# Optimization experiments

Measured on AMD Instinct MI355X. Metric: run time of the kernel, lower is better.

## Reference

```python
import jax, jax.numpy as jnp
import numpy as np

K = 2  # top-k experts per token

def setup_inputs() -> dict:
    key = jax.random.key(0)
    ks = jax.random.split(key, 4)
    B, D, E, H = 8192, 512, 8, 2048
    x = jax.random.normal(ks[0], (B, D), dtype=jnp.float32)
    w_gate = jax.random.normal(ks[1], (D, E), dtype=jnp.float32) * 0.02
    W1 = jax.random.normal(ks[2], (E, D, H), dtype=jnp.float32) * (1.0 / np.sqrt(D))
    b1 = jnp.zeros((E, H), dtype=jnp.float32)
    W2 = jax.random.normal(ks[3], (E, H, D), dtype=jnp.float32) * (1.0 / np.sqrt(H))
    b2 = jnp.zeros((E, D), dtype=jnp.float32)
    return {"x": x, "w_gate": w_gate, "W1": W1, "b1": b1, "W2": W2, "b2": b2}

def reference(x, w_gate, W1, b1, W2, b2):
    B, E = x.shape[0], w_gate.shape[1]
    # --- gating (eval path: clean logits, no noise) ---
    logits = x @ w_gate                                  # [B, E]
    top_vals, top_idx = jax.lax.top_k(logits, K)         # [B, K]
    top_gates = jax.nn.softmax(top_vals, axis=-1)        # softmax over top-k logits
    rows = jnp.arange(B)[:, None]
    gates = jnp.zeros((B, E), dtype=x.dtype).at[rows, top_idx].set(top_gates)  # [B, E]
    # --- expert MLPs (grouped GEMMs) ---
    h = jax.nn.gelu(jnp.einsum('bd,edh->beh', x, W1) + b1[None], approximate=False)  # [B, E, H]
    out = jnp.einsum('beh,ehd->bed', h, W2) + b2[None]   # [B, E, D]
    # --- combine weighted by sparse gates ---
    y = jnp.einsum('be,bed->bd', gates, out)             # [B, D]
    return y
```

## Files before the change

### kernel.cpp

```cpp
#include <hip/hip_runtime.h>
#include <cstdint>

#define B_TOK 8192
#define DIM   512
#define NEXP  8
#define HID   2048

#define BM 128
#define BN 128
#define BK 64
#define BN2 64
#define MAXTILES (B_TOK * 2 / BM + NEXP)
#define MPX 17
#define PAD_SLOTS (MAXTILES * BM)

typedef float  floatx4 __attribute__((ext_vector_type(4)));
typedef __bf16 bf16x8  __attribute__((ext_vector_type(8)));

__device__ __forceinline__ unsigned short f2bf(float f){
  unsigned u = __float_as_uint(f);
  u += 0x7fffu + ((u >> 16) & 1u);
  return (unsigned short)(u >> 16);
}

__device__ __forceinline__ float bf2f(unsigned short u){
  return __uint_as_float((unsigned)u << 16);
}

__device__ __forceinline__ float erf_fast(float x){
  float ax = fabsf(x);
  float t  = 1.0f / (1.0f + 0.3275911f * ax);
  float p  = t * (0.254829592f + t * (-0.284496736f + t * (1.421413741f +
             t * (-1.453152027f + t * 1.061405429f))));
  float r  = 1.0f - p * __expf(-ax * ax);
  return copysignf(r, x);
}

__device__ __forceinline__ float gelu_fast(float v){
  return 0.5f * v * (1.0f + erf_fast(v * 0.70710678118654752440f));
}

__device__ __forceinline__ void async_load16(const void* g, void* l){
  __builtin_amdgcn_global_load_lds(
      (__attribute__((address_space(1))) unsigned int*)const_cast<void*>(g),
      (__attribute__((address_space(3))) unsigned int*)l, 16, 0, 0);
}


__global__ void k_cvt_x(const float* __restrict__ x, unsigned short* __restrict__ xb){
  int i = blockIdx.x * blockDim.x + threadIdx.x;
  float4 v = ((const float4*)x)[i];
  ushort4 o;
  o.x = f2bf(v.x); o.y = f2bf(v.y); o.z = f2bf(v.z); o.w = f2bf(v.w);
  ((ushort4*)xb)[i] = o;
}

__global__ __launch_bounds__(256)
void k_transpose_bf16(const float* __restrict__ src, unsigned short* __restrict__ dst,
                      int R, int C){
  __shared__ unsigned short tile[64][65];
  const size_t eoff = (size_t)blockIdx.z * (size_t)R * (size_t)C;
  const float* s = src + eoff;
  unsigned short* d = dst + eoff;
  int r0 = blockIdx.y * 64, c0 = blockIdx.x * 64;
  int tr = threadIdx.x >> 4, tc = threadIdx.x & 15;
  #pragma unroll
  for (int i = 0; i < 4; i++){
    int r = tr + i * 16;
    float4 v = *(const float4*)(s + (size_t)(r0 + r) * C + c0 + tc * 4);
    tile[tc*4+0][r] = f2bf(v.x);
    tile[tc*4+1][r] = f2bf(v.y);
    tile[tc*4+2][r] = f2bf(v.z);
    tile[tc*4+3][r] = f2bf(v.w);
  }
  __syncthreads();
  #pragma unroll
  for (int i = 0; i < 4; i++){
    int rr = tr + i * 16;
    ushort4 o;
    o.x = tile[rr][tc*4+0]; o.y = tile[rr][tc*4+1];
    o.z = tile[rr][tc*4+2]; o.w = tile[rr][tc*4+3];
    *(ushort4*)(d + (size_t)(c0 + rr) * R + r0 + tc * 4) = o;
  }
}

__global__ __launch_bounds__(256)
void k_gate(const float* __restrict__ x, const float* __restrict__ wg,
            int* __restrict__ tidx, float* __restrict__ tgate){
  const int wave = threadIdx.x >> 6, lane = threadIdx.x & 63;
  const int t = blockIdx.x * 4 + wave;
  const float* xr = x + (size_t)t * DIM;
  double acc[8];
  #pragma unroll
  for (int e = 0; e < 8; e++) acc[e] = 0.0;
  for (int d = lane; d < DIM; d += 64){
    double xv = (double)xr[d];
    float4 a = *(const float4*)(wg + d * 8);
    float4 b = *(const float4*)(wg + d * 8 + 4);
    acc[0] += xv * (double)a.x; acc[1] += xv * (double)a.y;
    acc[2] += xv * (double)a.z; acc[3] += xv * (double)a.w;
    acc[4] += xv * (double)b.x; acc[5] += xv * (double)b.y;
    acc[6] += xv * (double)b.z; acc[7] += xv * (double)b.w;
  }
  #pragma unroll
  for (int off = 32; off > 0; off >>= 1){
    #pragma unroll
    for (int e = 0; e < 8; e++)
      acc[e] += __shfl_down(acc[e], off);
  }
  if (lane == 0){
    int i0 = 0; double v0 = acc[0];
    #pragma unroll
    for (int e = 1; e < 8; e++) if (acc[e] > v0){ v0 = acc[e]; i0 = e; }
    int i1 = -1; double v1 = -1e300;
    #pragma unroll
    for (int e = 0; e < 8; e++) if (e != i0 && acc[e] > v1){ v1 = acc[e]; i1 = e; }
    double g0 = 1.0 / (1.0 + exp(v1 - v0));
    tidx[2*t]   = i0; tidx[2*t+1] = i1;
    tgate[2*t]  = (float)g0;
    tgate[2*t+1]= (float)(1.0 - g0);
  }
}

__global__ __launch_bounds__(1024)
void k_count(const int* __restrict__ tidx, int* __restrict__ ctrl,
             int2* __restrict__ tmap){
  __shared__ int hist[16][8];
  const int tid = threadIdx.x;
  const int wave = tid >> 6;
  if (tid < 128) ((int*)hist)[tid] = 0;
  __syncthreads();
  #pragma unroll
  for (int i = 0; i < 8; i++){
    int t = i * 1024 + tid;
    int2 e = ((const int2*)tidx)[t];
    atomicAdd(&hist[wave][e.x], 1);
    atomicAdd(&hist[wave][e.y], 1);
  }
  __syncthreads();
  if (tid == 0){
    int o = 0, nt = 0;
    for (int e = 0; e < 8; e++){
      int c = 0;
      for (int w = 0; w < 16; w++) c += hist[w][e];
      ctrl[e] = c; ctrl[8 + e] = o; ctrl[16 + e] = o;
      int tiles = (c + BM - 1) / BM;
      for (int tk = 0; tk < tiles; tk++) tmap[nt++] = make_int2(e, tk * BM);
      o += tiles * BM;
    }
    for (; nt < MAXTILES; nt++) tmap[nt] = make_int2(0, 1 << 30);
  }
}

__global__ __launch_bounds__(256)
void k_place(const int* __restrict__ tidx, int* __restrict__ ctrl,
             int* __restrict__ perm, int2* __restrict__ slotpos){
  __shared__ int cnt[8];
  __shared__ int base[8];
  const int tid = threadIdx.x;
  if (tid < 8) cnt[tid] = 0;
  __syncthreads();
  const int t = blockIdx.x * 256 + tid;
  const int e0 = tidx[2*t], e1 = tidx[2*t+1];
  const int r0 = atomicAdd(&cnt[e0], 1);
  const int r1 = atomicAdd(&cnt[e1], 1);
  __syncthreads();
  if (tid < 8) base[tid] = atomicAdd(&ctrl[16 + tid], cnt[tid]);
  __syncthreads();
  const int p0 = base[e0] + r0, p1 = base[e1] + r1;
  perm[p0] = t;
  perm[p1] = t;
  slotpos[t] = make_int2(p0, p1);
}


__global__ __launch_bounds__(256, 4)
void k_gemm1(const unsigned short* __restrict__ xb,
             const unsigned short* __restrict__ w1t,
             const float* __restrict__ b1,
             unsigned short* __restrict__ h,
             const int* __restrict__ perm,
             const int* __restrict__ ctrl,
             const int2* __restrict__ tmap){
  const int xcd = blockIdx.x & 7;
  const int g   = blockIdx.x >> 3;
  const int nti = g & 15;
  const int mi  = g >> 4;
  const int2 tm = tmap[xcd * MPX + mi];
  const int e = tm.x;
  const int m0 = tm.y;
  const int count = ctrl[e];
  if (m0 >= count) return;
  const int hoff = ctrl[8 + e];
  const int n0 = nti * BN;

  __shared__ unsigned short smem[BM*BK + BN*BK + 2048];
  unsigned short* As = smem;
  unsigned short* Bs = smem + BM*BK;

  const int tid  = threadIdx.x;
  const int wave = tid >> 6;
  const int lane = tid & 63;
  const int rl   = wave * 32 + (lane >> 3);
  const int swz  = (lane & 7) ^ ((lane >> 3) & 7);

  const unsigned short* agp[4];
  const unsigned short* bgp[4];
  const unsigned short* w1e = w1t + (size_t)e * HID * DIM;
  #pragma unroll
  for (int i = 0; i < 4; i++){
    int srow = perm[hoff + m0 + rl + i * 8];
    agp[i] = xb + (size_t)srow * DIM + swz * 8;
    bgp[i] = w1e + (size_t)(n0 + rl + i * 8) * DIM + swz * 8;
  }
  unsigned short* asw = As + (wave * 32) * BK + lane * 8;
  unsigned short* bsw = Bs + (wave * 32) * BK + lane * 8;

  const int mh = (wave & 1) * 64;
  const int nh = (wave >> 1) * 64;
  const int fr = lane & 15;
  const int fq = lane >> 4;

  floatx4 acc[4][4];
  floatx4 zero = {0.f, 0.f, 0.f, 0.f};
  #pragma unroll
  for (int i = 0; i < 4; i++)
    #pragma unroll
    for (int j = 0; j < 4; j++) acc[i][j] = zero;

  for (int kt = 0; kt < DIM / BK; ++kt){
    #pragma unroll
    for (int i = 0; i < 4; i++){
      async_load16(agp[i] + kt * BK, asw + i * 8 * BK);
      async_load16(bgp[i] + kt * BK, bsw + i * 8 * BK);
    }
    __syncthreads();
    #pragma unroll
    for (int ks = 0; ks < 2; ks++){
      bf16x8 af[4], bfv[4];
      int kc = ks * 4 + fq;
      #pragma unroll
      for (int i = 0; i < 4; i++){
        int row = mh + i * 16 + fr;
        af[i] = *(const bf16x8*)(As + row * BK + ((kc ^ (row & 7)) << 3));
      }
      #pragma unroll
      for (int j = 0; j < 4; j++){
        int row = nh + j * 16 + fr;
        bfv[j] = *(const bf16x8*)(Bs + row * BK + ((kc ^ (row & 7)) << 3));
      }
      #pragma unroll
      for (int i = 0; i < 4; i++)
        #pragma unroll
        for (int j = 0; j < 4; j++)
          acc[i][j] = __builtin_amdgcn_mfma_f32_16x16x32_bf16(af[i], bfv[j], acc[i][j], 0, 0, 0);
    }
    __syncthreads();
  }

  unsigned short* wr = smem + wave * 4608;
  const int cm = fq * 4;
  const float* b1e = b1 + e * HID;
  #pragma unroll
  for (int i = 0; i < 4; i++){
    #pragma unroll
    for (int j = 0; j < 4; j++){
      float bias = b1e[n0 + nh + j * 16 + fr];
      #pragma unroll
      for (int r = 0; r < 4; r++){
        float v = acc[i][j][r] + bias;
        wr[(i * 16 + cm + r) * 72 + j * 16 + fr] = f2bf(gelu_fast(v));
      }
    }
  }
  __syncthreads();
  #pragma unroll
  for (int it = 0; it < 8; ++it){
    int row = it * 8 + (lane >> 3);
    int mrow = m0 + mh + row;
    if (mrow < count){
      uint4 vv = *(const uint4*)(wr + row * 72 + (lane & 7) * 8);
      *(uint4*)(h + (size_t)(hoff + mrow) * HID + n0 + nh + (lane & 7) * 8) = vv;
    }
  }
}

__global__ __launch_bounds__(256, 4)
void k_gemm2(const unsigned short* __restrict__ h,
             const unsigned short* __restrict__ w2t,
             unsigned short* __restrict__ slots,
             const int* __restrict__ ctrl,
             const int2* __restrict__ tmap){
  const int xcd = blockIdx.x & 7;
  const int g   = blockIdx.x >> 3;
  const int nti = g & 7;
  const int mi  = g >> 3;
  const int2 tm = tmap[xcd * MPX + mi];
  const int e = tm.x;
  const int m0 = tm.y;
  const int count = ctrl[e];
  if (m0 >= count) return;
  const int hoff = ctrl[8 + e];
  const int n0 = nti * BN2;

  __shared__ unsigned short smem[BM*BK + BN2*BK];
  unsigned short* As = smem;
  unsigned short* Bs = smem + BM*BK;

  const int tid  = threadIdx.x;
  const int wave = tid >> 6;
  const int lane = tid & 63;
  const int rl   = wave * 32 + (lane >> 3);
  const int rlb  = wave * 16 + (lane >> 3);
  const int swz  = (lane & 7) ^ ((lane >> 3) & 7);

  const unsigned short* agp[4];
  const unsigned short* bgp[2];
  const unsigned short* w2e = w2t + (size_t)e * DIM * HID;
  #pragma unroll
  for (int i = 0; i < 4; i++){
    agp[i] = h + (size_t)(hoff + m0 + rl + i * 8) * HID + swz * 8;
  }
  #pragma unroll
  for (int i = 0; i < 2; i++){
    bgp[i] = w2e + (size_t)(n0 + rlb + i * 8) * HID + swz * 8;
  }
  unsigned short* asw = As + (wave * 32) * BK + lane * 8;
  unsigned short* bsw = Bs + (wave * 16) * BK + lane * 8;

  const int mh  = (wave & 1) * 64;
  const int nh2 = (wave >> 1) * 32;
  const int fr = lane & 15;
  const int fq = lane >> 4;

  floatx4 acc[4][2];
  floatx4 zero = {0.f, 0.f, 0.f, 0.f};
  #pragma unroll
  for (int i = 0; i < 4; i++)
    #pragma unroll
    for (int j = 0; j < 2; j++) acc[i][j] = zero;

  for (int kt = 0; kt < HID / BK; ++kt){
    #pragma unroll
    for (int i = 0; i < 4; i++)
      async_load16(agp[i] + kt * BK, asw + i * 8 * BK);
    #pragma unroll
    for (int i = 0; i < 2; i++)
      async_load16(bgp[i] + kt * BK, bsw + i * 8 * BK);
    __syncthreads();
    #pragma unroll
    for (int ks = 0; ks < 2; ks++){
      bf16x8 af[4], bfv[2];
      int kc = ks * 4 + fq;
      #pragma unroll
      for (int i = 0; i < 4; i++){
        int row = mh + i * 16 + fr;
        af[i] = *(const bf16x8*)(As + row * BK + ((kc ^ (row & 7)) << 3));
      }
      #pragma unroll
      for (int j = 0; j < 2; j++){
        int row = nh2 + j * 16 + fr;
        bfv[j] = *(const bf16x8*)(Bs + row * BK + ((kc ^ (row & 7)) << 3));
      }
      #pragma unroll
      for (int i = 0; i < 4; i++)
        #pragma unroll
        for (int j = 0; j < 2; j++)
          acc[i][j] = __builtin_amdgcn_mfma_f32_16x16x32_bf16(af[i], bfv[j], acc[i][j], 0, 0, 0);
    }
    __syncthreads();
  }

  const int cm = fq * 4;
  #pragma unroll
  for (int i = 0; i < 4; i++){
    #pragma unroll
    for (int r = 0; r < 4; r++){
      int mrow = m0 + mh + i * 16 + cm + r;
      if (mrow < count){
        unsigned short* sr = slots + (size_t)(hoff + mrow) * DIM + n0 + nh2 + fr;
        sr[0]  = f2bf(acc[i][0][r]);
        sr[16] = f2bf(acc[i][1][r]);
      }
    }
  }
}

__global__ __launch_bounds__(256)
void k_combine(const unsigned short* __restrict__ slots, const int2* __restrict__ slotpos,
               const int* __restrict__ tidx, const float* __restrict__ tgate,
               const float* __restrict__ b2, float* __restrict__ y){
  const int idx = blockIdx.x * 256 + threadIdx.x;
  const int t  = idx >> 7;
  const int c4 = (idx & 127) * 4;
  int2 sp = slotpos[t];
  ushort4 u0 = *(const ushort4*)(slots + (size_t)sp.x * DIM + c4);
  ushort4 u1 = *(const ushort4*)(slots + (size_t)sp.y * DIM + c4);
  int   e0 = tidx[2*t],  e1 = tidx[2*t+1];
  float g0 = tgate[2*t], g1 = tgate[2*t+1];
  float4 bb0 = *(const float4*)(b2 + e0 * DIM + c4);
  float4 bb1 = *(const float4*)(b2 + e1 * DIM + c4);
  float4 r;
  r.x = g0 * (bf2f(u0.x) + bb0.x) + g1 * (bf2f(u1.x) + bb1.x);
  r.y = g0 * (bf2f(u0.y) + bb0.y) + g1 * (bf2f(u1.y) + bb1.y);
  r.z = g0 * (bf2f(u0.z) + bb0.z) + g1 * (bf2f(u1.z) + bb1.z);
  r.w = g0 * (bf2f(u0.w) + bb0.w) + g1 * (bf2f(u1.w) + bb1.w);
  *(float4*)(y + (size_t)t * DIM + c4) = r;
}

extern "C" void kernel_launch(void* const* d_in, const int* in_sizes, int n_in,
                              void* d_out, int out_size, void* d_ws, size_t ws_size,
                              hipStream_t stream){
  const float* x  = (const float*)d_in[0];
  const float* wg = (const float*)d_in[1];
  const float* W1 = (const float*)d_in[2];
  const float* b1 = (const float*)d_in[3];
  const float* W2 = (const float*)d_in[4];
  const float* b2 = (const float*)d_in[5];
  float* y = (float*)d_out;

  char* ws = (char*)d_ws;
  size_t off = 0;
  auto alloc = [&](size_t bytes) -> void* {
    void* p = ws + off;
    off = (off + bytes + 255) & ~(size_t)255;
    return p;
  };
  unsigned short* xb   = (unsigned short*)alloc((size_t)B_TOK * DIM * 2);
  unsigned short* w1t  = (unsigned short*)alloc((size_t)NEXP * HID * DIM * 2);
  unsigned short* slots = (unsigned short*)ws;
  static_assert((size_t)PAD_SLOTS * DIM * 2 <= (size_t)B_TOK * DIM * 2 + (size_t)NEXP * HID * DIM * 2,
                "slots must fit in dead xb+w1t region");
  unsigned short* w2t  = (unsigned short*)alloc((size_t)NEXP * DIM * HID * 2);
  unsigned short* hbuf = (unsigned short*)alloc((size_t)PAD_SLOTS * HID * 2);
  int*   perm    = (int*)  alloc((size_t)PAD_SLOTS * 4);
  int2*  slotpos = (int2*) alloc((size_t)B_TOK * 8);
  int2*  tmap    = (int2*) alloc(MAXTILES * 8);
  int*   tidx  = (int*)  alloc(2 * B_TOK * 4);
  float* tgate = (float*)alloc(2 * B_TOK * 4);
  int*   ctrl  = (int*)  alloc(24 * 4);

  hipMemsetAsync(perm, 0, (size_t)PAD_SLOTS * 4, stream);

  k_cvt_x<<<B_TOK * DIM / (256 * 4), 256, 0, stream>>>(x, xb);
  k_transpose_bf16<<<dim3(HID / 64, DIM / 64, NEXP), 256, 0, stream>>>(W1, w1t, DIM, HID);
  k_transpose_bf16<<<dim3(DIM / 64, HID / 64, NEXP), 256, 0, stream>>>(W2, w2t, HID, DIM);
  k_gate<<<B_TOK / 4, 256, 0, stream>>>(x, wg, tidx, tgate);
  k_count<<<1, 1024, 0, stream>>>(tidx, ctrl, tmap);
  k_place<<<B_TOK / 256, 256, 0, stream>>>(tidx, ctrl, perm, slotpos);
  k_gemm1<<<MAXTILES * (HID / BN), 256, 0, stream>>>(xb, w1t, b1, hbuf, perm, ctrl, tmap);
  k_gemm2<<<MAXTILES * (DIM / BN2), 256, 0, stream>>>(hbuf, w2t, slots, ctrl, tmap);
  k_combine<<<B_TOK * DIM / 4 / 256, 256, 0, stream>>>(slots, slotpos, tidx, tgate, b2, y);
}
```

Measured before the change: 290.4 us.

## Fuse x bf16 cast into gate kernel and remap MFMA columns for vector stores

```diff
diff --git a/kernel.cpp b/kernel.cpp
--- a/kernel.cpp
+++ b/kernel.cpp
@@ -46,14 +46,6 @@
       (__attribute__((address_space(3))) unsigned int*)l, 16, 0, 0);
 }
 
-
-__global__ void k_cvt_x(const float* __restrict__ x, unsigned short* __restrict__ xb){
-  int i = blockIdx.x * blockDim.x + threadIdx.x;
-  float4 v = ((const float4*)x)[i];
-  ushort4 o;
-  o.x = f2bf(v.x); o.y = f2bf(v.y); o.z = f2bf(v.z); o.w = f2bf(v.w);
-  ((ushort4*)xb)[i] = o;
-}
 
 __global__ __launch_bounds__(256)
 void k_transpose_bf16(const float* __restrict__ src, unsigned short* __restrict__ dst,
@@ -86,21 +78,25 @@
 
 __global__ __launch_bounds__(256)
 void k_gate(const float* __restrict__ x, const float* __restrict__ wg,
-            int* __restrict__ tidx, float* __restrict__ tgate){
+            int* __restrict__ tidx, float* __restrict__ tgate,
+            unsigned short* __restrict__ xb){
   const int wave = threadIdx.x >> 6, lane = threadIdx.x & 63;
   const int t = blockIdx.x * 4 + wave;
   const float* xr = x + (size_t)t * DIM;
+  unsigned short* xbr = xb + (size_t)t * DIM;
   double acc[8];
   #pragma unroll
   for (int e = 0; e < 8; e++) acc[e] = 0.0;
   for (int d = lane; d < DIM; d += 64){
-    double xv = (double)xr[d];
+    float xv = xr[d];
+    xbr[d] = f2bf(xv);
+    double xd = (double)xv;
     float4 a = *(const float4*)(wg + d * 8);
     float4 b = *(const float4*)(wg + d * 8 + 4);
-    acc[0] += xv * (double)a.x; acc[1] += xv * (double)a.y;
-    acc[2] += xv * (double)a.z; acc[3] += xv * (double)a.w;
-    acc[4] += xv * (double)b.x; acc[5] += xv * (double)b.y;
-    acc[6] += xv * (double)b.z; acc[7] += xv * (double)b.w;
+    acc[0] += xd * (double)a.x; acc[1] += xd * (double)a.y;
+    acc[2] += xd * (double)a.z; acc[3] += xd * (double)a.w;
+    acc[4] += xd * (double)b.x; acc[5] += xd * (double)b.y;
+    acc[6] += xd * (double)b.z; acc[7] += xd * (double)b.w;
   }
   #pragma unroll
   for (int off = 32; off > 0; off >>= 1){
@@ -194,7 +190,7 @@
   const int hoff = ctrl[8 + e];
   const int n0 = nti * BN;
 
-  __shared__ unsigned short smem[BM*BK + BN*BK + 2048];
+  __shared__ unsigned short smem[BM*BK + BN*BK];
   unsigned short* As = smem;
   unsigned short* Bs = smem + BM*BK;
 
@@ -246,7 +242,7 @@
       }
       #pragma unroll
       for (int j = 0; j < 4; j++){
-        int row = nh + j * 16 + fr;
+        int row = nh + fr * 4 + j;
         bfv[j] = *(const bf16x8*)(Bs + row * BK + ((kc ^ (row & 7)) << 3));
       }
       #pragma unroll
@@ -258,29 +254,22 @@
     __syncthreads();
   }
 
-  unsigned short* wr = smem + wave * 4608;
   const int cm = fq * 4;
-  const float* b1e = b1 + e * HID;
-  #pragma unroll
-  for (int i = 0; i < 4; i++){
-    #pragma unroll
-    for (int j = 0; j < 4; j++){
-      float bias = b1e[n0 + nh + j * 16 + fr];
-      #pragma unroll
-      for (int r = 0; r < 4; r++){
-        float v = acc[i][j][r] + bias;
-        wr[(i * 16 + cm + r) * 72 + j * 16 + fr] = f2bf(gelu_fast(v));
-      }
-    }
-  }
-  __syncthreads();
-  #pragma unroll
-  for (int it = 0; it < 8; ++it){
-    int row = it * 8 + (lane >> 3);
-    int mrow = m0 + mh + row;
-    if (mrow < count){
-      uint4 vv = *(const uint4*)(wr + row * 72 + (lane & 7) * 8);
-      *(uint4*)(h + (size_t)(hoff + mrow) * HID + n0 + nh + (lane & 7) * 8) = vv;
+  const int cn = n0 + nh + fr * 4;
+  float4 bias = *(const float4*)(b1 + e * HID + cn);
+  #pragma unroll
+  for (int i = 0; i < 4; i++){
+    #pragma unroll
+    for (int r = 0; r < 4; r++){
+      int mrow = m0 + mh + i * 16 + cm + r;
+      if (mrow < count){
+        ushort4 o;
+        o.x = f2bf(gelu_fast(acc[i][0][r] + bias.x));
+        o.y = f2bf(gelu_fast(acc[i][1][r] + bias.y));
+        o.z = f2bf(gelu_fast(acc[i][2][r] + bias.z));
+        o.w = f2bf(gelu_fast(acc[i][3][r] + bias.w));
+        *(ushort4*)(h + (size_t)(hoff + mrow) * HID + cn) = o;
+      }
     }
   }
 }
@@ -359,7 +348,7 @@
       }
       #pragma unroll
       for (int j = 0; j < 2; j++){
-        int row = nh2 + j * 16 + fr;
+        int row = nh2 + fr * 2 + j;
         bfv[j] = *(const bf16x8*)(Bs + row * BK + ((kc ^ (row & 7)) << 3));
       }
       #pragma unroll
@@ -372,15 +361,15 @@
   }
 
   const int cm = fq * 4;
+  const int cn = n0 + nh2 + fr * 2;
   #pragma unroll
   for (int i = 0; i < 4; i++){
     #pragma unroll
     for (int r = 0; r < 4; r++){
       int mrow = m0 + mh + i * 16 + cm + r;
       if (mrow < count){
-        unsigned short* sr = slots + (size_t)(hoff + mrow) * DIM + n0 + nh2 + fr;
-        sr[0]  = f2bf(acc[i][0][r]);
-        sr[16] = f2bf(acc[i][1][r]);
+        unsigned pk = (unsigned)f2bf(acc[i][0][r]) | ((unsigned)f2bf(acc[i][1][r]) << 16);
+        *(unsigned*)(slots + (size_t)(hoff + mrow) * DIM + cn) = pk;
       }
     }
   }
@@ -442,10 +431,9 @@
 
   hipMemsetAsync(perm, 0, (size_t)PAD_SLOTS * 4, stream);
 
-  k_cvt_x<<<B_TOK * DIM / (256 * 4), 256, 0, stream>>>(x, xb);
   k_transpose_bf16<<<dim3(HID / 64, DIM / 64, NEXP), 256, 0, stream>>>(W1, w1t, DIM, HID);
   k_transpose_bf16<<<dim3(DIM / 64, HID / 64, NEXP), 256, 0, stream>>>(W2, w2t, HID, DIM);
-  k_gate<<<B_TOK / 4, 256, 0, stream>>>(x, wg, tidx, tgate);
+  k_gate<<<B_TOK / 4, 256, 0, stream>>>(x, wg, tidx, tgate, xb);
   k_count<<<1, 1024, 0, stream>>>(tidx, ctrl, tmap);
   k_place<<<B_TOK / 256, 256, 0, stream>>>(tidx, ctrl, perm, slotpos);
   k_gemm1<<<MAXTILES * (HID / BN), 256, 0, stream>>>(xb, w1t, b1, hbuf, perm, ctrl, tmap);
```

Measured after the change: 281.8 us. 1.03x faster.
